# Optimization experiments

Hardware: AMD Instinct MI355X
Metric: run time of the kernel (lower is better)

Reference implementation:

```python
import jax, jax.numpy as jnp
import numpy as np

DIM = 192
RC = 16
M = 64
LN_EPS = 1e-5
NORM_EPS = 1e-12


def _layernorm(x, g, b):
    mu = jnp.mean(x, axis=-1, keepdims=True)
    var = jnp.mean((x - mu) ** 2, axis=-1, keepdims=True)
    return (x - mu) / jnp.sqrt(var + LN_EPS) * g + b


def _l2norm(x):
    n = jnp.sqrt(jnp.sum(x * x, axis=-1, keepdims=True))
    return x / jnp.maximum(n, NORM_EPS)


def setup_inputs() -> dict:
    key = jax.random.key(0)
    ks = jax.random.split(key, 12)
    B, N = 8, 16384
    s_q = 1.0 / np.sqrt(DIM)
    inp = {
        "x": jax.random.normal(ks[0], (B, N, DIM), jnp.float32),
        "dict_tokens": jax.random.normal(ks[1], (B, M, DIM), jnp.float32),
        "H": 128,
        "W": 128,
        "wq_w": jax.random.normal(ks[2], (DIM, RC), jnp.float32) * s_q,
        "wq_b": jnp.zeros((RC,), jnp.float32),
        "wk_w": jax.random.normal(ks[3], (DIM, RC), jnp.float32) * s_q,
        "wk_b": jnp.zeros((RC,), jnp.float32),
        "wv_w": jax.random.normal(ks[4], (DIM, DIM), jnp.float32) * s_q,
        "wv_b": jnp.zeros((DIM,), jnp.float32),
        "qn_g": jnp.ones((RC,), jnp.float32),
        "qn_b": jnp.zeros((RC,), jnp.float32),
        "kn_g": jnp.ones((RC,), jnp.float32),
        "kn_b": jnp.zeros((RC,), jnp.float32),
        "conv_w": jax.random.normal(ks[5], (DIM, 1, 3, 3), jnp.float32) / 3.0,
        "conv_b": jnp.zeros((DIM,), jnp.float32),
        "temperature": jnp.ones((1,), jnp.float32),
    }
    return inp


def reference(x, dict_tokens, H, W, wq_w, wq_b, wk_w, wk_b, wv_w, wv_b,
              qn_g, qn_b, kn_g, kn_b, conv_w, conv_b, temperature):
    # q: (B,N,rc), k: (B,M,rc)
    q = _l2norm(_layernorm(x @ wq_w + wq_b, qn_g, qn_b))
    k = _l2norm(_layernorm(dict_tokens @ wk_w + wk_b, kn_g, kn_b))
    # cosine-similarity attention with clamped temperature
    attn = jnp.einsum("bnr,bmr->bnm", q, k) / jnp.maximum(temperature, 0.5)
    attn = jax.nn.softmax(attn, axis=-1)
    # value + depthwise-conv refinement over the M token axis (Mx1 image)
    v = dict_tokens @ wv_w + wv_b                       # (B,M,C)
    v_img = jnp.transpose(v, (0, 2, 1))[..., None]      # (B,C,M,1)
    v_img = jax.lax.conv_general_dilated(
        v_img, conv_w, window_strides=(1, 1), padding=((1, 1), (1, 1)),
        dimension_numbers=("NCHW", "OIHW", "NCHW"), feature_group_count=DIM)
    v_img = v_img + conv_b[None, :, None, None]
    v_img = jax.nn.gelu(v_img, approximate=False)
    v = jnp.transpose(v_img[..., 0], (0, 2, 1))         # (B,M,C)
    out = jnp.einsum("bnm,bmc->bnc", attn, v)           # (B,N,C)
    return out, attn
```

## Files before the change

kernel.cpp:

```cpp
#include <hip/hip_runtime.h>
#include <math.h>

#define B_   8
#define N_   16384
#define M_   64
#define C_   192
#define RC_  16
#define AT_S 68

#define FMA4(acc, s, v) \
    acc.x = fmaf(s, v.x, acc.x); acc.y = fmaf(s, v.y, acc.y); \
    acc.z = fmaf(s, v.z, acc.z); acc.w = fmaf(s, v.w, acc.w)

__global__ __launch_bounds__(256) void k_prep_kernel(
    const float* __restrict__ dict,
    const float* __restrict__ wv_w, const float* __restrict__ wv_b,
    const float* __restrict__ conv_w, const float* __restrict__ conv_b,
    const float* __restrict__ wk_w, const float* __restrict__ wk_b,
    const float* __restrict__ kn_g, const float* __restrict__ kn_b,
    float* __restrict__ ws_vg, float* __restrict__ ws_k)
{
    const int b   = blockIdx.x >> 6;
    const int m   = blockIdx.x & 63;
    const int tid = threadIdx.x;
    const float* d0 = dict + (b * M_ + m) * C_;

    if (tid < 192) {
        const int c = tid;
        const bool hm = (m > 0), hp = (m < M_ - 1);
        const float* dm = hm ? d0 - C_ : d0;
        const float* dp = hp ? d0 + C_ : d0;
        float am = 0.f, ac = 0.f, ap = 0.f;
        #pragma unroll 4
        for (int d = 0; d < C_; ++d) {
            const float w = wv_w[d * C_ + c];
            am = fmaf(dm[d], w, am);
            ac = fmaf(d0[d], w, ac);
            ap = fmaf(dp[d], w, ap);
        }
        const float bia = wv_b[c];
        const float up = hm ? (am + bia) : 0.f;
        const float ct = ac + bia;
        const float dn = hp ? (ap + bia) : 0.f;
        float t = conv_b[c];
        t = fmaf(up, conv_w[c*9 + 1], t);
        t = fmaf(ct, conv_w[c*9 + 4], t);
        t = fmaf(dn, conv_w[c*9 + 7], t);
        ws_vg[(b * M_ + m) * C_ + c] = 0.5f * t * (1.0f + erff(t * 0.70710678118654752f));
    } else if (tid < 196) {
        const int j4 = tid - 192;
        const int c0 = j4 * 4;
        float a0 = wk_b[c0+0], a1 = wk_b[c0+1], a2 = wk_b[c0+2], a3 = wk_b[c0+3];
        #pragma unroll 4
        for (int d4 = 0; d4 < C_/4; ++d4) {
            const float4 xv = ((const float4*)d0)[d4];
            const float4 w0 = *(const float4*)&wk_w[(d4*4+0)*RC_ + c0];
            const float4 w1 = *(const float4*)&wk_w[(d4*4+1)*RC_ + c0];
            const float4 w2 = *(const float4*)&wk_w[(d4*4+2)*RC_ + c0];
            const float4 w3 = *(const float4*)&wk_w[(d4*4+3)*RC_ + c0];
            a0 = fmaf(xv.x, w0.x, a0); a1 = fmaf(xv.x, w0.y, a1); a2 = fmaf(xv.x, w0.z, a2); a3 = fmaf(xv.x, w0.w, a3);
            a0 = fmaf(xv.y, w1.x, a0); a1 = fmaf(xv.y, w1.y, a1); a2 = fmaf(xv.y, w1.z, a2); a3 = fmaf(xv.y, w1.w, a3);
            a0 = fmaf(xv.z, w2.x, a0); a1 = fmaf(xv.z, w2.y, a1); a2 = fmaf(xv.z, w2.z, a2); a3 = fmaf(xv.z, w2.w, a3);
            a0 = fmaf(xv.w, w3.x, a0); a1 = fmaf(xv.w, w3.y, a1); a2 = fmaf(xv.w, w3.z, a2); a3 = fmaf(xv.w, w3.w, a3);
        }
        float s  = a0 + a1 + a2 + a3;
        float ss = a0*a0 + a1*a1 + a2*a2 + a3*a3;
        s  += __shfl_xor(s, 1);  s  += __shfl_xor(s, 2);
        ss += __shfl_xor(ss, 1); ss += __shfl_xor(ss, 2);
        const float mu   = s * (1.0f/16.0f);
        const float var  = ss * (1.0f/16.0f) - mu*mu;
        const float rstd = rsqrtf(var + 1e-5f);
        const float4 g4 = *(const float4*)&kn_g[c0];
        const float4 b4 = *(const float4*)&kn_b[c0];
        const float y0 = (a0 - mu) * rstd * g4.x + b4.x;
        const float y1 = (a1 - mu) * rstd * g4.y + b4.y;
        const float y2 = (a2 - mu) * rstd * g4.z + b4.z;
        const float y3 = (a3 - mu) * rstd * g4.w + b4.w;
        float n2 = y0*y0 + y1*y1 + y2*y2 + y3*y3;
        n2 += __shfl_xor(n2, 1); n2 += __shfl_xor(n2, 2);
        const float inv = 1.0f / fmaxf(sqrtf(n2), 1e-12f);
        float4 o; o.x = y0*inv; o.y = y1*inv; o.z = y2*inv; o.w = y3*inv;
        *(float4*)&ws_k[(b * M_ + m) * RC_ + c0] = o;
    }
}

__global__ __launch_bounds__(256, 2) void k_main_kernel(
    const float* __restrict__ x, const float* __restrict__ ws_k,
    const float* __restrict__ ws_vg,
    const float* __restrict__ wq_w, const float* __restrict__ wq_b,
    const float* __restrict__ qn_g, const float* __restrict__ qn_b,
    const float* __restrict__ temp,
    float* __restrict__ out, float* __restrict__ attn_out)
{
    __shared__ float vg_s[M_ * C_];
    __shared__ float k_s[M_ * RC_];
    __shared__ float attn_t[M_ * AT_S];

    const int tid   = threadIdx.x;
    const int b     = blockIdx.x >> 8;
    const int n0    = (blockIdx.x & 255) * M_;
    const int lane  = tid & 63;
    const int lbase = lane & ~3;

    float4 st[12]; float4 kst;
    {
        const float4* vgb4 = (const float4*)(ws_vg + b * (M_ * C_));
        #pragma unroll
        for (int i = 0; i < 12; ++i) st[i] = vgb4[tid + 256 * i];
        kst = ((const float4*)(ws_k + b * (M_ * RC_)))[tid];
    }

    const int r  = tid >> 2;
    const int j4 = tid & 3;
    const int c0 = j4 * 4;

    const float* xr = x + (size_t)(b * N_ + n0 + r) * C_;
    float a0 = wq_b[c0+0], a1 = wq_b[c0+1], a2 = wq_b[c0+2], a3 = wq_b[c0+3];
    #pragma unroll 4
    for (int d4 = 0; d4 < C_/4; ++d4) {
        const float4 xv = ((const float4*)xr)[d4];
        const float4 w0 = *(const float4*)&wq_w[(d4*4+0)*RC_ + c0];
        const float4 w1 = *(const float4*)&wq_w[(d4*4+1)*RC_ + c0];
        const float4 w2 = *(const float4*)&wq_w[(d4*4+2)*RC_ + c0];
        const float4 w3 = *(const float4*)&wq_w[(d4*4+3)*RC_ + c0];
        a0 = fmaf(xv.x, w0.x, a0); a1 = fmaf(xv.x, w0.y, a1); a2 = fmaf(xv.x, w0.z, a2); a3 = fmaf(xv.x, w0.w, a3);
        a0 = fmaf(xv.y, w1.x, a0); a1 = fmaf(xv.y, w1.y, a1); a2 = fmaf(xv.y, w1.z, a2); a3 = fmaf(xv.y, w1.w, a3);
        a0 = fmaf(xv.z, w2.x, a0); a1 = fmaf(xv.z, w2.y, a1); a2 = fmaf(xv.z, w2.z, a2); a3 = fmaf(xv.z, w2.w, a3);
        a0 = fmaf(xv.w, w3.x, a0); a1 = fmaf(xv.w, w3.y, a1); a2 = fmaf(xv.w, w3.z, a2); a3 = fmaf(xv.w, w3.w, a3);
    }
    float4 q[4];
    {
        float s  = a0 + a1 + a2 + a3;
        float ss = a0*a0 + a1*a1 + a2*a2 + a3*a3;
        s  += __shfl_xor(s, 1);  s  += __shfl_xor(s, 2);
        ss += __shfl_xor(ss, 1); ss += __shfl_xor(ss, 2);
        const float mu   = s * (1.0f/16.0f);
        const float var  = ss * (1.0f/16.0f) - mu*mu;
        const float rstd = rsqrtf(var + 1e-5f);
        const float4 g4 = *(const float4*)&qn_g[c0];
        const float4 b4 = *(const float4*)&qn_b[c0];
        const float y0 = (a0 - mu) * rstd * g4.x + b4.x;
        const float y1 = (a1 - mu) * rstd * g4.y + b4.y;
        const float y2 = (a2 - mu) * rstd * g4.z + b4.z;
        const float y3 = (a3 - mu) * rstd * g4.w + b4.w;
        float n2 = y0*y0 + y1*y1 + y2*y2 + y3*y3;
        n2 += __shfl_xor(n2, 1); n2 += __shfl_xor(n2, 2);
        const float inv = 1.0f / fmaxf(sqrtf(n2), 1e-12f);
        float4 o; o.x = y0*inv; o.y = y1*inv; o.z = y2*inv; o.w = y3*inv;
        #pragma unroll
        for (int j = 0; j < 4; ++j) {
            q[j].x = __shfl(o.x, lbase + j);
            q[j].y = __shfl(o.y, lbase + j);
            q[j].z = __shfl(o.z, lbase + j);
            q[j].w = __shfl(o.w, lbase + j);
        }
    }
    const float tinv = 1.0f / fmaxf(temp[0], 0.5f);

    {
        #pragma unroll
        for (int i = 0; i < 12; ++i) ((float4*)vg_s)[tid + 256 * i] = st[i];
        ((float4*)k_s)[tid] = kst;
    }
    __syncthreads();

    {
        float sc[16];
        #pragma unroll
        for (int mm = 0; mm < 16; ++mm) {
            const int m = mm*4 + j4;
            const float4 k0 = *(const float4*)&k_s[m*RC_ + 0];
            const float4 k1 = *(const float4*)&k_s[m*RC_ + 4];
            const float4 k2 = *(const float4*)&k_s[m*RC_ + 8];
            const float4 k3 = *(const float4*)&k_s[m*RC_ + 12];
            float d = q[0].x*k0.x;
            d = fmaf(q[0].y, k0.y, d); d = fmaf(q[0].z, k0.z, d); d = fmaf(q[0].w, k0.w, d);
            d = fmaf(q[1].x, k1.x, d); d = fmaf(q[1].y, k1.y, d); d = fmaf(q[1].z, k1.z, d); d = fmaf(q[1].w, k1.w, d);
            d = fmaf(q[2].x, k2.x, d); d = fmaf(q[2].y, k2.y, d); d = fmaf(q[2].z, k2.z, d); d = fmaf(q[2].w, k2.w, d);
            d = fmaf(q[3].x, k3.x, d); d = fmaf(q[3].y, k3.y, d); d = fmaf(q[3].z, k3.z, d); d = fmaf(q[3].w, k3.w, d);
            sc[mm] = d * tinv;
        }
        float mx = sc[0];
        #pragma unroll
        for (int mm = 1; mm < 16; ++mm) mx = fmaxf(mx, sc[mm]);
        mx = fmaxf(mx, __shfl_xor(mx, 1)); mx = fmaxf(mx, __shfl_xor(mx, 2));
        float es = 0.0f;
        #pragma unroll
        for (int mm = 0; mm < 16; ++mm) { sc[mm] = expf(sc[mm] - mx); es += sc[mm]; }
        es += __shfl_xor(es, 1); es += __shfl_xor(es, 2);
        const float einv = 1.0f / es;
        float* aw = attn_out + (size_t)(b * N_ + n0 + r) * M_;
        #pragma unroll
        for (int mm = 0; mm < 16; ++mm) {
            const float p = sc[mm] * einv;
            attn_t[(mm*4 + j4)*AT_S + r] = p;
            aw[mm*4 + j4] = p;
        }
    }
    __syncthreads();

    {
        const int rq = tid >> 4;
        const int cq = tid & 15;
        float4 ac0[3], ac1[3], ac2[3], ac3[3];
        #pragma unroll
        for (int t = 0; t < 3; ++t) {
            ac0[t] = make_float4(0.f,0.f,0.f,0.f);
            ac1[t] = make_float4(0.f,0.f,0.f,0.f);
            ac2[t] = make_float4(0.f,0.f,0.f,0.f);
            ac3[t] = make_float4(0.f,0.f,0.f,0.f);
        }
        #pragma unroll 4
        for (int m = 0; m < M_; ++m) {
            const float4 av = *(const float4*)&attn_t[m*AT_S + rq*4];
            const float4* vr = (const float4*)(vg_s + m*C_ + cq*12);
            #pragma unroll
            for (int t = 0; t < 3; ++t) {
                const float4 v = vr[t];
                FMA4(ac0[t], av.x, v);
                FMA4(ac1[t], av.y, v);
                FMA4(ac2[t], av.z, v);
                FMA4(ac3[t], av.w, v);
            }
        }
        float* o0 = out + (size_t)(b * N_ + n0 + rq*4) * C_ + cq*12;
        #pragma unroll
        for (int t = 0; t < 3; ++t) {
            *(float4*)&o0[t*4]          = ac0[t];
            *(float4*)&o0[C_   + t*4]   = ac1[t];
            *(float4*)&o0[2*C_ + t*4]   = ac2[t];
            *(float4*)&o0[3*C_ + t*4]   = ac3[t];
        }
    }
}

extern "C" void kernel_launch(void* const* d_in, const int* in_sizes, int n_in,
                              void* d_out, int out_size, void* d_ws, size_t ws_size,
                              hipStream_t stream) {
    const float* x      = (const float*)d_in[0];
    const float* dict   = (const float*)d_in[1];
    const float* wq_w   = (const float*)d_in[4];
    const float* wq_b   = (const float*)d_in[5];
    const float* wk_w   = (const float*)d_in[6];
    const float* wk_b   = (const float*)d_in[7];
    const float* wv_w   = (const float*)d_in[8];
    const float* wv_b   = (const float*)d_in[9];
    const float* qn_g   = (const float*)d_in[10];
    const float* qn_b   = (const float*)d_in[11];
    const float* kn_g   = (const float*)d_in[12];
    const float* kn_b   = (const float*)d_in[13];
    const float* conv_w = (const float*)d_in[14];
    const float* conv_b = (const float*)d_in[15];
    const float* temp   = (const float*)d_in[16];

    float* out  = (float*)d_out;
    float* attn = out + (size_t)B_ * N_ * C_;

    float* ws_vg = (float*)d_ws;
    float* ws_k  = ws_vg + B_ * M_ * C_;

    k_prep_kernel<<<B_ * M_,        256, 0, stream>>>(dict, wv_w, wv_b, conv_w, conv_b,
                                                      wk_w, wk_b, kn_g, kn_b, ws_vg, ws_k);
    k_main_kernel<<<B_ * (N_ / M_), 256, 0, stream>>>(x, ws_k, ws_vg, wq_w, wq_b,
                                                      qn_g, qn_b, temp, out, attn);
}
```

Baseline: 343.9 us.

## Broadcast softmax probabilities via wave shuffles and double rows per block

Removes the shared-memory attention transpose buffer and its extra barrier. Each wave now takes its probabilities straight from registers with __shfl in the attn@V loop, so a wave computes the output for its own 16 rows. Blocks grow to 512 threads covering 128 rows, which halves the per-row cost of loading the value tile into LDS. The trade-off is four shuffles per m iteration, and a fully unrolled m loop that adds register pressure under the 512,4 launch bounds.

```diff
diff --git a/kernel.cpp b/kernel.cpp
--- a/kernel.cpp
+++ b/kernel.cpp
@@ -6,7 +6,7 @@
 #define M_   64
 #define C_   192
 #define RC_  16
-#define AT_S 68
+#define ROWS 128
 
 #define FMA4(acc, s, v) \
     acc.x = fmaf(s, v.x, acc.x); acc.y = fmaf(s, v.y, acc.y); \
@@ -84,7 +84,7 @@
     }
 }
 
-__global__ __launch_bounds__(256, 2) void k_main_kernel(
+__global__ __launch_bounds__(512, 4) void k_main_kernel(
     const float* __restrict__ x, const float* __restrict__ ws_k,
     const float* __restrict__ ws_vg,
     const float* __restrict__ wq_w, const float* __restrict__ wq_b,
@@ -94,20 +94,19 @@
 {
     __shared__ float vg_s[M_ * C_];
     __shared__ float k_s[M_ * RC_];
-    __shared__ float attn_t[M_ * AT_S];
 
     const int tid   = threadIdx.x;
-    const int b     = blockIdx.x >> 8;
-    const int n0    = (blockIdx.x & 255) * M_;
+    const int b     = blockIdx.x >> 7;
+    const int n0    = (blockIdx.x & 127) * ROWS;
     const int lane  = tid & 63;
     const int lbase = lane & ~3;
 
-    float4 st[12]; float4 kst;
+    float4 st[6]; float4 kst;
     {
         const float4* vgb4 = (const float4*)(ws_vg + b * (M_ * C_));
         #pragma unroll
-        for (int i = 0; i < 12; ++i) st[i] = vgb4[tid + 256 * i];
-        kst = ((const float4*)(ws_k + b * (M_ * RC_)))[tid];
+        for (int i = 0; i < 6; ++i) st[i] = vgb4[tid + 512 * i];
+        if (tid < 256) kst = ((const float4*)(ws_k + b * (M_ * RC_)))[tid];
     }
 
     const int r  = tid >> 2;
@@ -159,13 +158,13 @@
 
     {
         #pragma unroll
-        for (int i = 0; i < 12; ++i) ((float4*)vg_s)[tid + 256 * i] = st[i];
-        ((float4*)k_s)[tid] = kst;
+        for (int i = 0; i < 6; ++i) ((float4*)vg_s)[tid + 512 * i] = st[i];
+        if (tid < 256) ((float4*)k_s)[tid] = kst;
     }
     __syncthreads();
 
-    {
-        float sc[16];
+    float sc[16];
+    {
         #pragma unroll
         for (int mm = 0; mm < 16; ++mm) {
             const int m = mm*4 + j4;
@@ -192,16 +191,18 @@
         float* aw = attn_out + (size_t)(b * N_ + n0 + r) * M_;
         #pragma unroll
         for (int mm = 0; mm < 16; ++mm) {
-            const float p = sc[mm] * einv;
-            attn_t[(mm*4 + j4)*AT_S + r] = p;
-            aw[mm*4 + j4] = p;
-        }
-    }
-    __syncthreads();
-
-    {
-        const int rq = tid >> 4;
-        const int cq = tid & 15;
+            sc[mm] *= einv;
+            aw[mm*4 + j4] = sc[mm];
+        }
+    }
+
+    {
+        const int w0lane = tid & 63;
+        const int rql = w0lane >> 4;
+        const int cq  = w0lane & 15;
+        const int wv  = tid >> 6;
+        const int bl  = rql * 16;
+
         float4 ac0[3], ac1[3], ac2[3], ac3[3];
         #pragma unroll
         for (int t = 0; t < 3; ++t) {
@@ -210,20 +211,24 @@
             ac2[t] = make_float4(0.f,0.f,0.f,0.f);
             ac3[t] = make_float4(0.f,0.f,0.f,0.f);
         }
-        #pragma unroll 4
+        #pragma unroll
         for (int m = 0; m < M_; ++m) {
-            const float4 av = *(const float4*)&attn_t[m*AT_S + rq*4];
+            const float p0 = __shfl(sc[m >> 2], bl + 0  + (m & 3));
+            const float p1 = __shfl(sc[m >> 2], bl + 4  + (m & 3));
+            const float p2 = __shfl(sc[m >> 2], bl + 8  + (m & 3));
+            const float p3 = __shfl(sc[m >> 2], bl + 12 + (m & 3));
             const float4* vr = (const float4*)(vg_s + m*C_ + cq*12);
             #pragma unroll
             for (int t = 0; t < 3; ++t) {
                 const float4 v = vr[t];
-                FMA4(ac0[t], av.x, v);
-                FMA4(ac1[t], av.y, v);
-                FMA4(ac2[t], av.z, v);
-                FMA4(ac3[t], av.w, v);
+                FMA4(ac0[t], p0, v);
+                FMA4(ac1[t], p1, v);
+                FMA4(ac2[t], p2, v);
+                FMA4(ac3[t], p3, v);
             }
         }
-        float* o0 = out + (size_t)(b * N_ + n0 + rq*4) * C_ + cq*12;
+        const int row0 = 16*wv + 4*rql;
+        float* o0 = out + (size_t)(b * N_ + n0 + row0) * C_ + cq*12;
         #pragma unroll
         for (int t = 0; t < 3; ++t) {
             *(float4*)&o0[t*4]          = ac0[t];
@@ -259,8 +264,8 @@
     float* ws_vg = (float*)d_ws;
     float* ws_k  = ws_vg + B_ * M_ * C_;
 
-    k_prep_kernel<<<B_ * M_,        256, 0, stream>>>(dict, wv_w, wv_b, conv_w, conv_b,
-                                                      wk_w, wk_b, kn_g, kn_b, ws_vg, ws_k);
-    k_main_kernel<<<B_ * (N_ / M_), 256, 0, stream>>>(x, ws_k, ws_vg, wq_w, wq_b,
-                                                      qn_g, qn_b, temp, out, attn);
+    k_prep_kernel<<<B_ * M_,          256, 0, stream>>>(dict, wv_w, wv_b, conv_w, conv_b,
+                                                        wk_w, wk_b, kn_g, kn_b, ws_vg, ws_k);
+    k_main_kernel<<<B_ * (N_ / ROWS), 512, 0, stream>>>(x, ws_k, ws_vg, wq_w, wq_b,
+                                                        qn_g, qn_b, temp, out, attn);
 }
```

Result: slower. 382.6 us (+11.3%).

## Stage wq in LDS, split q-projection over reduction dim, drop second barrier

Applied to the files above, without the earlier changes.

The Q projection now loads wq_w into shared memory (padded rows) and has each of the four lanes per row cover a quarter of the input dimension for all 16 outputs, then reduces with shuffles, so x reads become coalesced across lanes. The attention tile reuses the same shared buffer, and each wave now consumes only the attention rows it wrote itself, which removes one __syncthreads. The value and key staging becomes a direct global-to-LDS copy instead of a register prefetch. The cost is more registers per thread (16 accumulators), more shuffles, and a loss of the earlier overlap between the value-tile load and the projection.

```diff
diff --git a/kernel.cpp b/kernel.cpp
--- a/kernel.cpp
+++ b/kernel.cpp
@@ -6,7 +6,8 @@
 #define M_   64
 #define C_   192
 #define RC_  16
-#define AT_S 68
+#define CW   20
+#define ATS  68
 
 #define FMA4(acc, s, v) \
     acc.x = fmaf(s, v.x, acc.x); acc.y = fmaf(s, v.y, acc.y); \
@@ -94,74 +95,77 @@
 {
     __shared__ float vg_s[M_ * C_];
     __shared__ float k_s[M_ * RC_];
-    __shared__ float attn_t[M_ * AT_S];
-
-    const int tid   = threadIdx.x;
-    const int b     = blockIdx.x >> 8;
-    const int n0    = (blockIdx.x & 255) * M_;
-    const int lane  = tid & 63;
-    const int lbase = lane & ~3;
-
-    float4 st[12]; float4 kst;
+    __shared__ float u_s[M_ * ATS];
+
+    const int tid  = threadIdx.x;
+    const int b    = blockIdx.x >> 8;
+    const int n0   = (blockIdx.x & 255) * M_;
+    const int lane = tid & 63;
+    const int r    = tid >> 2;
+    const int j4   = tid & 3;
+    const int wv   = tid >> 6;
+
     {
         const float4* vgb4 = (const float4*)(ws_vg + b * (M_ * C_));
         #pragma unroll
-        for (int i = 0; i < 12; ++i) st[i] = vgb4[tid + 256 * i];
-        kst = ((const float4*)(ws_k + b * (M_ * RC_)))[tid];
-    }
-
-    const int r  = tid >> 2;
-    const int j4 = tid & 3;
-    const int c0 = j4 * 4;
-
-    const float* xr = x + (size_t)(b * N_ + n0 + r) * C_;
-    float a0 = wq_b[c0+0], a1 = wq_b[c0+1], a2 = wq_b[c0+2], a3 = wq_b[c0+3];
-    #pragma unroll 4
-    for (int d4 = 0; d4 < C_/4; ++d4) {
-        const float4 xv = ((const float4*)xr)[d4];
-        const float4 w0 = *(const float4*)&wq_w[(d4*4+0)*RC_ + c0];
-        const float4 w1 = *(const float4*)&wq_w[(d4*4+1)*RC_ + c0];
-        const float4 w2 = *(const float4*)&wq_w[(d4*4+2)*RC_ + c0];
-        const float4 w3 = *(const float4*)&wq_w[(d4*4+3)*RC_ + c0];
-        a0 = fmaf(xv.x, w0.x, a0); a1 = fmaf(xv.x, w0.y, a1); a2 = fmaf(xv.x, w0.z, a2); a3 = fmaf(xv.x, w0.w, a3);
-        a0 = fmaf(xv.y, w1.x, a0); a1 = fmaf(xv.y, w1.y, a1); a2 = fmaf(xv.y, w1.z, a2); a3 = fmaf(xv.y, w1.w, a3);
-        a0 = fmaf(xv.z, w2.x, a0); a1 = fmaf(xv.z, w2.y, a1); a2 = fmaf(xv.z, w2.z, a2); a3 = fmaf(xv.z, w2.w, a3);
-        a0 = fmaf(xv.w, w3.x, a0); a1 = fmaf(xv.w, w3.y, a1); a2 = fmaf(xv.w, w3.z, a2); a3 = fmaf(xv.w, w3.w, a3);
-    }
-    float4 q[4];
-    {
-        float s  = a0 + a1 + a2 + a3;
-        float ss = a0*a0 + a1*a1 + a2*a2 + a3*a3;
-        s  += __shfl_xor(s, 1);  s  += __shfl_xor(s, 2);
-        ss += __shfl_xor(ss, 1); ss += __shfl_xor(ss, 2);
+        for (int i = 0; i < 12; ++i)
+            ((float4*)vg_s)[tid + 256 * i] = vgb4[tid + 256 * i];
+        ((float4*)k_s)[tid] = ((const float4*)(ws_k + b * (M_ * RC_)))[tid];
+        #pragma unroll
+        for (int i = 0; i < 3; ++i) {
+            const int idx = tid + 256 * i;
+            const float4 w = ((const float4*)wq_w)[idx];
+            *(float4*)&u_s[(idx >> 2) * CW + (idx & 3) * 4] = w;
+        }
+    }
+    __syncthreads();
+
+    const float4* xr4 = (const float4*)(x + (size_t)(b * N_ + n0 + r) * C_);
+    float acc[16];
+    #pragma unroll
+    for (int c = 0; c < 16; ++c) acc[c] = 0.f;
+    #pragma unroll
+    for (int i = 0; i < 12; ++i) {
+        const float4 xv = xr4[i*4 + j4];
+        const float* wr = &u_s[(i*16 + j4*4) * CW];
+        #define WROW(xd, row) { \
+            const float4 w0 = *(const float4*)&wr[(row)*CW + 0]; \
+            const float4 w1 = *(const float4*)&wr[(row)*CW + 4]; \
+            const float4 w2 = *(const float4*)&wr[(row)*CW + 8]; \
+            const float4 w3 = *(const float4*)&wr[(row)*CW + 12]; \
+            acc[0]=fmaf(xd,w0.x,acc[0]); acc[1]=fmaf(xd,w0.y,acc[1]); acc[2]=fmaf(xd,w0.z,acc[2]); acc[3]=fmaf(xd,w0.w,acc[3]); \
+            acc[4]=fmaf(xd,w1.x,acc[4]); acc[5]=fmaf(xd,w1.y,acc[5]); acc[6]=fmaf(xd,w1.z,acc[6]); acc[7]=fmaf(xd,w1.w,acc[7]); \
+            acc[8]=fmaf(xd,w2.x,acc[8]); acc[9]=fmaf(xd,w2.y,acc[9]); acc[10]=fmaf(xd,w2.z,acc[10]); acc[11]=fmaf(xd,w2.w,acc[11]); \
+            acc[12]=fmaf(xd,w3.x,acc[12]); acc[13]=fmaf(xd,w3.y,acc[13]); acc[14]=fmaf(xd,w3.z,acc[14]); acc[15]=fmaf(xd,w3.w,acc[15]); }
+        WROW(xv.x, 0) WROW(xv.y, 1) WROW(xv.z, 2) WROW(xv.w, 3)
+        #undef WROW
+    }
+    float qv[16];
+    {
+        #pragma unroll
+        for (int c = 0; c < 16; ++c) {
+            acc[c] += __shfl_xor(acc[c], 1);
+            acc[c] += __shfl_xor(acc[c], 2);
+            acc[c] += wq_b[c];
+        }
+        float s = 0.f, ss = 0.f;
+        #pragma unroll
+        for (int c = 0; c < 16; ++c) { s += acc[c]; ss += acc[c]*acc[c]; }
         const float mu   = s * (1.0f/16.0f);
         const float var  = ss * (1.0f/16.0f) - mu*mu;
         const float rstd = rsqrtf(var + 1e-5f);
-        const float4 g4 = *(const float4*)&qn_g[c0];
-        const float4 b4 = *(const float4*)&qn_b[c0];
-        const float y0 = (a0 - mu) * rstd * g4.x + b4.x;
-        const float y1 = (a1 - mu) * rstd * g4.y + b4.y;
-        const float y2 = (a2 - mu) * rstd * g4.z + b4.z;
-        const float y3 = (a3 - mu) * rstd * g4.w + b4.w;
-        float n2 = y0*y0 + y1*y1 + y2*y2 + y3*y3;
-        n2 += __shfl_xor(n2, 1); n2 += __shfl_xor(n2, 2);
+        float n2 = 0.f;
+        #pragma unroll
+        for (int c = 0; c < 16; ++c) {
+            const float y = (acc[c] - mu) * rstd * qn_g[c] + qn_b[c];
+            qv[c] = y; n2 += y*y;
+        }
         const float inv = 1.0f / fmaxf(sqrtf(n2), 1e-12f);
-        float4 o; o.x = y0*inv; o.y = y1*inv; o.z = y2*inv; o.w = y3*inv;
-        #pragma unroll
-        for (int j = 0; j < 4; ++j) {
-            q[j].x = __shfl(o.x, lbase + j);
-            q[j].y = __shfl(o.y, lbase + j);
-            q[j].z = __shfl(o.z, lbase + j);
-            q[j].w = __shfl(o.w, lbase + j);
-        }
+        #pragma unroll
+        for (int c = 0; c < 16; ++c) qv[c] *= inv;
     }
     const float tinv = 1.0f / fmaxf(temp[0], 0.5f);
 
-    {
-        #pragma unroll
-        for (int i = 0; i < 12; ++i) ((float4*)vg_s)[tid + 256 * i] = st[i];
-        ((float4*)k_s)[tid] = kst;
-    }
     __syncthreads();
 
     {
@@ -173,11 +177,11 @@
             const float4 k1 = *(const float4*)&k_s[m*RC_ + 4];
             const float4 k2 = *(const float4*)&k_s[m*RC_ + 8];
             const float4 k3 = *(const float4*)&k_s[m*RC_ + 12];
-            float d = q[0].x*k0.x;
-            d = fmaf(q[0].y, k0.y, d); d = fmaf(q[0].z, k0.z, d); d = fmaf(q[0].w, k0.w, d);
-            d = fmaf(q[1].x, k1.x, d); d = fmaf(q[1].y, k1.y, d); d = fmaf(q[1].z, k1.z, d); d = fmaf(q[1].w, k1.w, d);
-            d = fmaf(q[2].x, k2.x, d); d = fmaf(q[2].y, k2.y, d); d = fmaf(q[2].z, k2.z, d); d = fmaf(q[2].w, k2.w, d);
-            d = fmaf(q[3].x, k3.x, d); d = fmaf(q[3].y, k3.y, d); d = fmaf(q[3].z, k3.z, d); d = fmaf(q[3].w, k3.w, d);
+            float d = qv[0]*k0.x;
+            d = fmaf(qv[1], k0.y, d); d = fmaf(qv[2], k0.z, d); d = fmaf(qv[3], k0.w, d);
+            d = fmaf(qv[4], k1.x, d); d = fmaf(qv[5], k1.y, d); d = fmaf(qv[6], k1.z, d); d = fmaf(qv[7], k1.w, d);
+            d = fmaf(qv[8], k2.x, d); d = fmaf(qv[9], k2.y, d); d = fmaf(qv[10], k2.z, d); d = fmaf(qv[11], k2.w, d);
+            d = fmaf(qv[12], k3.x, d); d = fmaf(qv[13], k3.y, d); d = fmaf(qv[14], k3.z, d); d = fmaf(qv[15], k3.w, d);
             sc[mm] = d * tinv;
         }
         float mx = sc[0];
@@ -193,15 +197,14 @@
         #pragma unroll
         for (int mm = 0; mm < 16; ++mm) {
             const float p = sc[mm] * einv;
-            attn_t[(mm*4 + j4)*AT_S + r] = p;
             aw[mm*4 + j4] = p;
-        }
-    }
-    __syncthreads();
-
-    {
-        const int rq = tid >> 4;
-        const int cq = tid & 15;
+            u_s[(mm*4 + j4)*ATS + r] = p;
+        }
+    }
+
+    {
+        const int rql = lane >> 4;
+        const int cq  = lane & 15;
         float4 ac0[3], ac1[3], ac2[3], ac3[3];
         #pragma unroll
         for (int t = 0; t < 3; ++t) {
@@ -212,7 +215,7 @@
         }
         #pragma unroll 4
         for (int m = 0; m < M_; ++m) {
-            const float4 av = *(const float4*)&attn_t[m*AT_S + rq*4];
+            const float4 av = *(const float4*)&u_s[m*ATS + 16*wv + 4*rql];
             const float4* vr = (const float4*)(vg_s + m*C_ + cq*12);
             #pragma unroll
             for (int t = 0; t < 3; ++t) {
@@ -223,13 +226,14 @@
                 FMA4(ac3[t], av.w, v);
             }
         }
-        float* o0 = out + (size_t)(b * N_ + n0 + rq*4) * C_ + cq*12;
+        const int row0 = 16*wv + 4*rql;
+        float* o0 = out + (size_t)(b * N_ + n0 + row0) * C_ + cq*12;
         #pragma unroll
         for (int t = 0; t < 3; ++t) {
-            *(float4*)&o0[t*4]          = ac0[t];
-            *(float4*)&o0[C_   + t*4]   = ac1[t];
-            *(float4*)&o0[2*C_ + t*4]   = ac2[t];
-            *(float4*)&o0[3*C_ + t*4]   = ac3[t];
+            *(float4*)&o0[t*4]        = ac0[t];
+            *(float4*)&o0[C_   + t*4] = ac1[t];
+            *(float4*)&o0[2*C_ + t*4] = ac2[t];
+            *(float4*)&o0[3*C_ + t*4] = ac3[t];
         }
     }
 }
```

Result: faster. 300.4 us (-12.6%).
